# Performance work log

Measured on AMD Instinct MI355X. Metric: run time of the kernel, lower is better.

The kernel has to match this reference:

```python
import jax, jax.numpy as jnp
import numpy as np

H, KV, D = 12, 4, 128  # n_head, n_kv_head, head_dim
VE_GATE_CH = 12

def _rmsnorm(x):
    eps = jnp.finfo(x.dtype).eps  # matches torch F.rms_norm default eps
    return x * jax.lax.rsqrt(jnp.mean(x * x, axis=-1, keepdims=True) + eps)

def _rope(x, cos, sin):
    d = x.shape[-1] // 2
    x1, x2 = x[..., :d], x[..., d:]
    return jnp.concatenate([x1 * cos + x2 * sin, -x1 * sin + x2 * cos], axis=-1)

def setup_inputs() -> dict:
    key = jax.random.key(0)
    ks = jax.random.split(key, 9)
    B, T, C = 2, 2048, 1536
    x = jax.random.normal(ks[0], (B, T, C), jnp.float32)
    ve = jax.random.normal(ks[1], (B, T, KV * D), jnp.float32)
    ang = jax.random.uniform(ks[2], (1, T, 1, D // 2), jnp.float32) * (2.0 * np.pi)
    cos, sin = jnp.cos(ang), jnp.sin(ang)
    Wq = jax.random.normal(ks[3], (H * D, C), jnp.float32) * 0.02
    Wk = jax.random.normal(ks[4], (KV * D, C), jnp.float32) * 0.02
    Wv = jax.random.normal(ks[5], (KV * D, C), jnp.float32) * 0.02
    Wproj = jax.random.normal(ks[6], (C, C), jnp.float32) * 0.02
    Wg = jax.random.normal(ks[7], (KV, VE_GATE_CH), jnp.float32) * 0.02
    return dict(x=x, ve=ve, cos=cos, sin=sin, Wq=Wq, Wk=Wk, Wv=Wv, Wproj=Wproj, Wg=Wg, window=1024)

def reference(x, ve, cos, sin, Wq, Wk, Wv, Wproj, Wg, window):
    B, T, C = x.shape
    q = (x @ Wq.T).reshape(B, T, H, D)
    k = (x @ Wk.T).reshape(B, T, KV, D)
    v = (x @ Wv.T).reshape(B, T, KV, D)
    # value-embedding gate: 3*sigmoid(Linear(x[..., :12])) per kv head
    gate = 3.0 * jax.nn.sigmoid(x[..., :VE_GATE_CH] @ Wg.T)  # [B,T,KV]
    v = v + gate[..., None] * ve.reshape(B, T, KV, D)
    q = _rmsnorm(_rope(q, cos, sin)) * 1.2
    k = _rmsnorm(_rope(k, cos, sin)) * 1.2
    rep = H // KV  # GQA group size
    qh = q.transpose(0, 2, 1, 3).reshape(B, KV, rep, T, D)
    kh = k.transpose(0, 2, 1, 3)  # [B,KV,T,D]
    vh = v.transpose(0, 2, 1, 3)
    scores = jnp.einsum('bgrtd,bgsd->bgrts', qh, kh) / np.sqrt(D)
    row = jnp.arange(T)[:, None]
    col = jnp.arange(T)[None, :]
    if window < 0 or window >= T:
        mask = col <= row  # pure causal
    else:
        mask = (col <= row) & (row - col <= window)  # causal sliding window
    scores = jnp.where(mask, scores, -jnp.inf)
    att = jax.nn.softmax(scores, axis=-1)
    y = jnp.einsum('bgrts,bgsd->bgrtd', att, vh)
    y = y.reshape(B, H, T, D).transpose(0, 2, 1, 3).reshape(B, T, H * D)
    return y @ Wproj.T
```

## Files before the change

### kernel.cpp

```cpp
#include <hip/hip_runtime.h>
#include <hip/hip_bf16.h>
#include <math.h>

#define B_  2
#define T_  2048
#define C_  1536
#define H_  12
#define KV_ 4
#define D_  128
#define M_  (B_*T_)
#define REP_ (H_/KV_)
#define NQKV_ 2560

typedef __bf16 bf16x8 __attribute__((ext_vector_type(8)));
typedef float  f32x4  __attribute__((ext_vector_type(4)));
typedef unsigned u32x4 __attribute__((ext_vector_type(4)));

union BCast { u32x4 u; bf16x8 b; };

__device__ inline bf16x8 ldb8(const ushort* p) {
    BCast c; c.u = *reinterpret_cast<const u32x4*>(p); return c.b;
}

__device__ inline ushort f2bf(float f) {
    union { float f; unsigned u; } v; v.f = f;
    unsigned u = v.u;
    return (ushort)((u + 0x7FFF + ((u >> 16) & 1)) >> 16);
}

__device__ inline float bf2f(ushort u) {
    union { unsigned u; float f; } v; v.u = (unsigned)u << 16;
    return v.f;
}

__device__ inline void async_copy16(const ushort* g, ushort* l) {
    __builtin_amdgcn_global_load_lds(
        (const __attribute__((address_space(1))) unsigned*)g,
        (__attribute__((address_space(3))) unsigned*)l, 16, 0, 0);
}

__device__ __host__ inline int dperm(int d) {
    return (d < 32) ? d : (d < 64 ? d + 32 : (d < 96 ? d - 32 : d));
}

template<bool BF16OUT>
__global__ __launch_bounds__(256) void gemm_bf16_bt(const ushort* __restrict__ A,
                                                    const ushort* __restrict__ Bm,
                                                    void* __restrict__ Cp,
                                                    int M, int N, int K) {
    __shared__ ushort As[128 * 32];
    __shared__ ushort Bs[128 * 32];
    const int tid  = threadIdx.x;
    const int wave = tid >> 6, lane = tid & 63;
    const int m16 = lane & 15, quad = lane >> 4;
    const int bm = blockIdx.y * 128, bn = blockIdx.x * 128;
    const int wm = (wave >> 1) * 64, wn = (wave & 1) * 64;

    const int lrow = lane >> 2;
    const int lcol = (lane & 3) * 8;
    const ushort* Ag = A  + (size_t)(bm + wave * 16 + lrow) * K + lcol;
    const ushort* Bg = Bm + (size_t)(bn + wave * 16 + lrow) * K + lcol;
    ushort* AsW0 = As + wave * 512;
    ushort* AsW1 = As + 2048 + wave * 512;
    ushort* BsW0 = Bs + wave * 512;
    ushort* BsW1 = Bs + 2048 + wave * 512;
    const size_t rowskip = (size_t)64 * K;

    f32x4 acc[4][4];
    #pragma unroll
    for (int i = 0; i < 4; i++)
        #pragma unroll
        for (int j = 0; j < 4; j++) acc[i][j] = (f32x4){0.f, 0.f, 0.f, 0.f};

    for (int k0 = 0; k0 < K; k0 += 32) {
        async_copy16(Ag + k0,           AsW0);
        async_copy16(Ag + k0 + rowskip, AsW1);
        async_copy16(Bg + k0,           BsW0);
        async_copy16(Bg + k0 + rowskip, BsW1);
        __syncthreads();

        bf16x8 af[4], bfr[4];
        #pragma unroll
        for (int i = 0; i < 4; i++)
            af[i] = ldb8(As + (wm + i * 16 + m16) * 32 + quad * 8);
        #pragma unroll
        for (int j = 0; j < 4; j++)
            bfr[j] = ldb8(Bs + (wn + j * 16 + m16) * 32 + quad * 8);
        #pragma unroll
        for (int i = 0; i < 4; i++)
            #pragma unroll
            for (int j = 0; j < 4; j++)
                acc[i][j] = __builtin_amdgcn_mfma_f32_16x16x32_bf16(af[i], bfr[j], acc[i][j], 0, 0, 0);
        __syncthreads();
    }

    #pragma unroll
    for (int i = 0; i < 4; i++) {
        #pragma unroll
        for (int reg = 0; reg < 4; reg++) {
            const int row = bm + wm + i * 16 + quad * 4 + reg;
            if constexpr (BF16OUT) {
                ushort* C = (ushort*)Cp;
                #pragma unroll
                for (int j = 0; j < 4; j++)
                    C[(size_t)row * N + bn + wn + j * 16 + m16] = f2bf(acc[i][j][reg]);
            } else {
                float* C = (float*)Cp;
                #pragma unroll
                for (int j = 0; j < 4; j++)
                    C[(size_t)row * N + bn + wn + j * 16 + m16] = acc[i][j][reg];
            }
        }
    }
}

#define KQ_ 1536
__global__ __launch_bounds__(256) void gemm_qkv(const ushort* __restrict__ A,
                                                const ushort* __restrict__ Bm,
                                                ushort* __restrict__ Qp,
                                                ushort* __restrict__ Kp,
                                                ushort* __restrict__ vbuf,
                                                const float* __restrict__ cosb,
                                                const float* __restrict__ sinb) {
    __shared__ ushort As[128 * 32];
    __shared__ ushort Bs[128 * 32];
    const int tid  = threadIdx.x;
    const int wave = tid >> 6, lane = tid & 63;
    const int m16 = lane & 15, quad = lane >> 4;
    const int bm = blockIdx.y * 128, bn = blockIdx.x * 128;
    const int wm = (wave >> 1) * 64, wn = (wave & 1) * 64;

    const int lrow = lane >> 2;
    const int lcol = (lane & 3) * 8;
    const ushort* Ag = A  + (size_t)(bm + wave * 16 + lrow) * KQ_ + lcol;
    const ushort* Bg = Bm + (size_t)(bn + wave * 16 + lrow) * KQ_ + lcol;
    ushort* AsW0 = As + wave * 512;
    ushort* AsW1 = As + 2048 + wave * 512;
    ushort* BsW0 = Bs + wave * 512;
    ushort* BsW1 = Bs + 2048 + wave * 512;
    const size_t rowskip = (size_t)64 * KQ_;

    f32x4 acc[4][4];
    #pragma unroll
    for (int i = 0; i < 4; i++)
        #pragma unroll
        for (int j = 0; j < 4; j++) acc[i][j] = (f32x4){0.f, 0.f, 0.f, 0.f};

    for (int k0 = 0; k0 < KQ_; k0 += 32) {
        async_copy16(Ag + k0,           AsW0);
        async_copy16(Ag + k0 + rowskip, AsW1);
        async_copy16(Bg + k0,           BsW0);
        async_copy16(Bg + k0 + rowskip, BsW1);
        __syncthreads();

        bf16x8 af[4], bfr[4];
        #pragma unroll
        for (int i = 0; i < 4; i++)
            af[i] = ldb8(As + (wm + i * 16 + m16) * 32 + quad * 8);
        #pragma unroll
        for (int j = 0; j < 4; j++)
            bfr[j] = ldb8(Bs + (wn + j * 16 + m16) * 32 + quad * 8);
        #pragma unroll
        for (int i = 0; i < 4; i++)
            #pragma unroll
            for (int j = 0; j < 4; j++)
                acc[i][j] = __builtin_amdgcn_mfma_f32_16x16x32_bf16(af[i], bfr[j], acc[i][j], 0, 0, 0);
        __syncthreads();
    }

    if (bn < 2048) {
        float* ssqS = (float*)As;
        float ssq[4][4];
        #pragma unroll
        for (int i = 0; i < 4; i++) {
            #pragma unroll
            for (int reg = 0; reg < 4; reg++) {
                float v = acc[i][0][reg]*acc[i][0][reg] + acc[i][1][reg]*acc[i][1][reg]
                        + acc[i][2][reg]*acc[i][2][reg] + acc[i][3][reg]*acc[i][3][reg];
                v += __shfl_xor(v, 1); v += __shfl_xor(v, 2);
                v += __shfl_xor(v, 4); v += __shfl_xor(v, 8);
                ssq[i][reg] = v;
            }
        }
        if (m16 == 0) {
            #pragma unroll
            for (int i = 0; i < 4; i++)
                #pragma unroll
                for (int reg = 0; reg < 4; reg++)
                    ssqS[(wm + i*16 + quad*4 + reg) * 2 + (wave & 1)] = ssq[i][reg];
        }
        __syncthreads();

        const bool isq = (bn < 1536);
        const float osc = isq ? (1.2f * 1.2f * 0.08838834764831845f) : 1.0f;
        const int hh  = isq ? (bn >> 7) : ((bn - 1536) >> 7);
        const int nh  = isq ? H_ : KV_;
        ushort* outp  = isq ? Qp : Kp;

        float scl[4][4];
        #pragma unroll
        for (int i = 0; i < 4; i++) {
            #pragma unroll
            for (int reg = 0; reg < 4; reg++) {
                const int r = wm + i*16 + quad*4 + reg;
                const float tot = ssqS[r*2] + ssqS[r*2 + 1];
                scl[i][reg] = rsqrtf(tot * (1.0f/128.0f) + 1.1920928955078125e-07f) * osc;
            }
        }

        #pragma unroll
        for (int i = 0; i < 4; i++) {
            #pragma unroll
            for (int reg = 0; reg < 4; reg++) {
                const int row = bm + wm + i*16 + quad*4 + reg;
                const int b = row >> 11, t = row & (T_ - 1);
                ushort* orow = outp + ((size_t)(b * nh + hh) * T_ + t) * D_;
                const float sc = scl[i][reg];
                #pragma unroll
                for (int jp = 0; jp < 2; jp++) {
                    const int ipair = (wn ? 32 : 0) + jp*16 + m16;
                    const float c = cosb[t*64 + ipair], s = sinb[t*64 + ipair];
                    const float x1 = acc[i][jp][reg], x2 = acc[i][jp+2][reg];
                    orow[wn + jp*16 + m16]       = f2bf((x1*c + x2*s) * sc);
                    orow[wn + (jp+2)*16 + m16]   = f2bf((x2*c - x1*s) * sc);
                }
            }
        }
    } else {
        const int cb = bn - 2048 + wn;
        #pragma unroll
        for (int i = 0; i < 4; i++) {
            #pragma unroll
            for (int reg = 0; reg < 4; reg++) {
                const int row = bm + wm + i*16 + quad*4 + reg;
                ushort* vr = vbuf + (size_t)row * 512 + cb + m16;
                #pragma unroll
                for (int j = 0; j < 4; j++)
                    vr[j*16] = f2bf(acc[i][j][reg]);
            }
        }
    }
}

#define SEG0 1572864
#define SEG1 2162688
#define SEG2 2359296
#define SEG3 2555904
#define SEG4 3145728
#define ROW4 384
__global__ __launch_bounds__(256) void cast_all(const float* __restrict__ x,
                                                const float* __restrict__ Wq,
                                                const float* __restrict__ Wk,
                                                const float* __restrict__ Wv,
                                                const float* __restrict__ Wp,
                                                ushort* __restrict__ xb,
                                                ushort* __restrict__ Wqkvb,
                                                ushort* __restrict__ Wpb) {
    const int i = blockIdx.x * 256 + threadIdx.x;
    float4 v; size_t dst4; ushort* dstp;
    if (i < SEG0) {
        v = ((const float4*)x)[i]; dstp = xb; dst4 = i;
    } else if (i < SEG1) {
        const int j = i - SEG0;
        const int r = j / ROW4, c4 = j - r * ROW4;
        const int d = r & 127, hh = r >> 7;
        v = ((const float4*)Wq)[j]; dstp = Wqkvb;
        dst4 = (size_t)(hh * 128 + dperm(d)) * ROW4 + c4;
    } else if (i < SEG2) {
        const int j = i - SEG1;
        const int r = j / ROW4, c4 = j - r * ROW4;
        const int d = r & 127, g = r >> 7;
        v = ((const float4*)Wk)[j]; dstp = Wqkvb;
        dst4 = (size_t)(1536 + g * 128 + dperm(d)) * ROW4 + c4;
    } else if (i < SEG3) {
        const int j = i - SEG2;
        v = ((const float4*)Wv)[j]; dstp = Wqkvb;
        dst4 = (size_t)2048 * ROW4 + j;
    } else {
        const int j = i - SEG3;
        v = ((const float4*)Wp)[j]; dstp = Wpb; dst4 = j;
    }
    ((ushort4*)dstp)[dst4] = make_ushort4(f2bf(v.x), f2bf(v.y), f2bf(v.z), f2bf(v.w));
}

__global__ __launch_bounds__(256) void gate_vt(const ushort* __restrict__ vbuf,
                                               const float* __restrict__ x,
                                               const float* __restrict__ ve,
                                               const float* __restrict__ Wg,
                                               ushort* __restrict__ Vt) {
    const int t0 = blockIdx.x * 64, g = blockIdx.y, b = blockIdx.z;
    __shared__ float gateS[64];
    __shared__ ushort tile[128][66];
    const int tid = threadIdx.x;
    if (tid < 64) {
        const float* xr = x + (size_t)(b * T_ + t0 + tid) * C_;
        float acc = 0.f;
        #pragma unroll
        for (int c = 0; c < 12; c++) acc += xr[c] * Wg[g * 12 + c];
        gateS[tid] = 3.0f / (1.0f + __expf(-acc));
    }
    __syncthreads();
    #pragma unroll
    for (int i = 0; i < 32; i++) {
        int idx = i * 256 + tid;
        int r = idx >> 7;
        int d = idx & 127;
        size_t offv = (size_t)(b * T_ + t0 + r) * 512 + g * D_ + d;
        tile[d][r] = f2bf(bf2f(vbuf[offv]) + gateS[r] * ve[offv]);
    }
    __syncthreads();
    ushort* ob = Vt + ((size_t)(b * KV_ + g) * D_) * T_ + t0;
    #pragma unroll
    for (int i = 0; i < 32; i++) {
        int idx = i * 256 + tid;
        int d = idx >> 6;
        int c = idx & 63;
        ob[(size_t)d * T_ + c] = tile[d][c];
    }
}

__global__ __launch_bounds__(256, 3) void attn_mfma(const ushort* __restrict__ Qp,
                                                    const ushort* __restrict__ Kp,
                                                    const ushort* __restrict__ Vt,
                                                    ushort* __restrict__ Y,
                                                    const int* __restrict__ wptr) {
    const int t0 = blockIdx.x * 64;
    const int h  = blockIdx.y, b = blockIdx.z;
    const int g  = h / REP_;
    const int tid  = threadIdx.x;
    const int wave = tid >> 6, lane = tid & 63;
    const int m16 = lane & 15, quad = lane >> 4;

    __shared__ ushort Ks[4 * 32 * 32];
    __shared__ ushort Vs[128 * 32];
    __shared__ ushort Pl[4][16 * 40];

    const int w = *wptr;
    const bool windowed = (w >= 0 && w < T_);
    const unsigned wu = windowed ? (unsigned)w : 0x7FFFFFFFu;
    int s_lo = 0;
    if (windowed) { s_lo = t0 - w; if (s_lo < 0) s_lo = 0; }
    const int s_hi = t0 + 63;
    const int ss0 = s_lo & ~31;
    const int tw = t0 + wave * 16;

    const ushort* qrow = Qp + ((size_t)(b * H_ + h) * T_ + tw + m16) * D_ + quad * 8;
    bf16x8 qa[4];
    #pragma unroll
    for (int kc = 0; kc < 4; kc++) qa[kc] = ldb8(qrow + kc * 32);

    const ushort* kbase = Kp + (size_t)(b * KV_ + g) * T_ * D_;
    const ushort* vbase = Vt + (size_t)(b * KV_ + g) * D_ * T_;

    const int c0 = wave, c1 = wave + 4;
    const ushort* kg0 = kbase + (size_t)((c0 & 1) * 16 + (lane >> 2)) * D_ + (c0 >> 1) * 32 + (lane & 3) * 8;
    const ushort* kg1 = kbase + (size_t)((c1 & 1) * 16 + (lane >> 2)) * D_ + (c1 >> 1) * 32 + (lane & 3) * 8;
    ushort* kl0 = Ks + c0 * 512;
    ushort* kl1 = Ks + c1 * 512;
    const ushort* vg0 = vbase + (size_t)(c0 * 16 + (lane >> 2)) * T_ + (lane & 3) * 8;
    const ushort* vg1 = vbase + (size_t)(c1 * 16 + (lane >> 2)) * T_ + (lane & 3) * 8;
    ushort* vl0 = Vs + c0 * 512;
    ushort* vl1 = Vs + c1 * 512;

    f32x4 o[8];
    #pragma unroll
    for (int dt = 0; dt < 8; dt++) o[dt] = (f32x4){0.f, 0.f, 0.f, 0.f};
    f32x4 lacc = (f32x4){0.f, 0.f, 0.f, 0.f};
    BCast onesc; onesc.u = (u32x4){0x3F803F80u, 0x3F803F80u, 0x3F803F80u, 0x3F803F80u};
    const bf16x8 ones = onesc.b;
    ushort* pw = &Pl[wave][0];

    for (int ss = ss0; ss <= s_hi; ss += 32) {
        const size_t koff = (size_t)ss * D_;
        async_copy16(kg0 + koff, kl0);
        async_copy16(kg1 + koff, kl1);
        async_copy16(vg0 + ss,   vl0);
        async_copy16(vg1 + ss,   vl1);
        __syncthreads();

        f32x4 s0 = (f32x4){0.f,0.f,0.f,0.f};
        f32x4 s1 = (f32x4){0.f,0.f,0.f,0.f};
        #pragma unroll
        for (int kc = 0; kc < 4; kc++) {
            bf16x8 kf0 = ldb8(Ks + kc * 1024 + m16 * 32 + quad * 8);
            bf16x8 kf1 = ldb8(Ks + kc * 1024 + (16 + m16) * 32 + quad * 8);
            s0 = __builtin_amdgcn_mfma_f32_16x16x32_bf16(qa[kc], kf0, s0, 0, 0, 0);
            s1 = __builtin_amdgcn_mfma_f32_16x16x32_bf16(qa[kc], kf1, s1, 0, 0, 0);
        }

        const int sA = ss + m16, sB = ss + 16 + m16;
        #pragma unroll
        for (int reg = 0; reg < 4; reg++) {
            const int t = tw + quad * 4 + reg;
            const float pa = ((unsigned)(t - sA) <= wu) ? __expf(s0[reg]) : 0.f;
            const float pb = ((unsigned)(t - sB) <= wu) ? __expf(s1[reg]) : 0.f;
            pw[(quad * 4 + reg) * 40 + m16]      = f2bf(pa);
            pw[(quad * 4 + reg) * 40 + 16 + m16] = f2bf(pb);
        }

        __builtin_amdgcn_s_waitcnt(0xc07f);
        bf16x8 pfrag = ldb8(pw + m16 * 40 + quad * 8);

        #pragma unroll
        for (int dt = 0; dt < 8; dt++) {
            bf16x8 vf = ldb8(Vs + (dt * 16 + m16) * 32 + quad * 8);
            o[dt] = __builtin_amdgcn_mfma_f32_16x16x32_bf16(pfrag, vf, o[dt], 0, 0, 0);
        }
        lacc = __builtin_amdgcn_mfma_f32_16x16x32_bf16(pfrag, ones, lacc, 0, 0, 0);
        __syncthreads();
    }

    float inv[4];
    #pragma unroll
    for (int reg = 0; reg < 4; reg++) inv[reg] = 1.0f / lacc[reg];
    ushort* yb = Y + ((size_t)(b * T_ + tw + quad * 4) * H_ + h) * D_ + m16;
    #pragma unroll
    for (int reg = 0; reg < 4; reg++)
        #pragma unroll
        for (int dt = 0; dt < 8; dt++)
            yb[(size_t)reg * H_ * D_ + dt * 16] = f2bf(o[dt][reg] * inv[reg]);
}

extern "C" void kernel_launch(void* const* d_in, const int* in_sizes, int n_in,
                              void* d_out, int out_size, void* d_ws, size_t ws_size,
                              hipStream_t stream) {
    const float* x     = (const float*)d_in[0];
    const float* ve    = (const float*)d_in[1];
    const float* cosb  = (const float*)d_in[2];
    const float* sinb  = (const float*)d_in[3];
    const float* Wq    = (const float*)d_in[4];
    const float* Wk    = (const float*)d_in[5];
    const float* Wv    = (const float*)d_in[6];
    const float* Wproj = (const float*)d_in[7];
    const float* Wg    = (const float*)d_in[8];
    const int*   wptr  = (const int*)d_in[9];
    float* out = (float*)d_out;

    ushort* xb    = (ushort*)d_ws;
    ushort* vbuf  = xb    + (size_t)M_ * C_;
    ushort* Qp    = vbuf  + (size_t)M_ * 512;
    ushort* Kp    = Qp    + (size_t)M_ * C_;
    ushort* Vt    = Kp    + (size_t)M_ * 512;
    ushort* yb16  = Vt    + (size_t)M_ * 512;
    ushort* Wqkvb = yb16  + (size_t)M_ * C_;
    ushort* Wpb   = Wqkvb + (size_t)NQKV_ * C_;

    cast_all<<<SEG4 / 256, 256, 0, stream>>>(x, Wq, Wk, Wv, Wproj, xb, Wqkvb, Wpb);

    gemm_qkv<<<dim3(NQKV_ / 128, M_ / 128), 256, 0, stream>>>(xb, Wqkvb, Qp, Kp, vbuf,
                                                              cosb, sinb);

    gate_vt<<<dim3(T_ / 64, KV_, B_), 256, 0, stream>>>(vbuf, x, ve, Wg, Vt);

    attn_mfma<<<dim3(T_ / 64, H_, B_), 256, 0, stream>>>(Qp, Kp, Vt, yb16, wptr);

    gemm_bf16_bt<false><<<dim3(C_ / 128, M_ / 128), 256, 0, stream>>>(yb16, Wpb, out, M_, C_, C_);
}
```

Measured before the change: 277.5 us.

## Move RoPE/RMSNorm out of QKV GEMM epilogue and double attention query tile

The QKV GEMM now writes raw bf16 Q and K without the row-norm reduction, barrier and RoPE in its epilogue. A new small kernel applies RoPE and RMSNorm to K in place. The attention kernel applies them to Q while loading it. Each attention wave now handles 32 query rows instead of 16, so every K/V tile staged in LDS is reused across twice the rows, with half the blocks. The costs are an extra launch plus a read-modify-write pass over K, Q normalization done on bf16-rounded values, and higher register pressure (launch bounds lowered from 3 to 2 blocks per SM).

Result: slower. 291.8 us (+5.1%).

```diff
diff --git a/kernel.cpp b/kernel.cpp
--- a/kernel.cpp
+++ b/kernel.cpp
@@ -16,7 +16,7 @@
 typedef float  f32x4  __attribute__((ext_vector_type(4)));
 typedef unsigned u32x4 __attribute__((ext_vector_type(4)));
 
-union BCast { u32x4 u; bf16x8 b; };
+union BCast { u32x4 u; bf16x8 b; ushort s[8]; };
 
 __device__ inline bf16x8 ldb8(const ushort* p) {
     BCast c; c.u = *reinterpret_cast<const u32x4*>(p); return c.b;
@@ -119,9 +119,7 @@
                                                 const ushort* __restrict__ Bm,
                                                 ushort* __restrict__ Qp,
                                                 ushort* __restrict__ Kp,
-                                                ushort* __restrict__ vbuf,
-                                                const float* __restrict__ cosb,
-                                                const float* __restrict__ sinb) {
+                                                ushort* __restrict__ vbuf) {
     __shared__ ushort As[128 * 32];
     __shared__ ushort Bs[128 * 32];
     const int tid  = threadIdx.x;
@@ -169,61 +167,20 @@
     }
 
     if (bn < 2048) {
-        float* ssqS = (float*)As;
-        float ssq[4][4];
+        const bool isq = (bn < 1536);
+        const int hh = isq ? (bn >> 7) : ((bn - 1536) >> 7);
+        const int nh = isq ? H_ : KV_;
+        ushort* outp = isq ? Qp : Kp;
         #pragma unroll
         for (int i = 0; i < 4; i++) {
             #pragma unroll
             for (int reg = 0; reg < 4; reg++) {
-                float v = acc[i][0][reg]*acc[i][0][reg] + acc[i][1][reg]*acc[i][1][reg]
-                        + acc[i][2][reg]*acc[i][2][reg] + acc[i][3][reg]*acc[i][3][reg];
-                v += __shfl_xor(v, 1); v += __shfl_xor(v, 2);
-                v += __shfl_xor(v, 4); v += __shfl_xor(v, 8);
-                ssq[i][reg] = v;
-            }
-        }
-        if (m16 == 0) {
-            #pragma unroll
-            for (int i = 0; i < 4; i++)
+                const int row = bm + wm + i * 16 + quad * 4 + reg;
+                const int b = row >> 11, t = row & (T_ - 1);
+                ushort* orow = outp + ((size_t)(b * nh + hh) * T_ + t) * D_ + wn + m16;
                 #pragma unroll
-                for (int reg = 0; reg < 4; reg++)
-                    ssqS[(wm + i*16 + quad*4 + reg) * 2 + (wave & 1)] = ssq[i][reg];
-        }
-        __syncthreads();
-
-        const bool isq = (bn < 1536);
-        const float osc = isq ? (1.2f * 1.2f * 0.08838834764831845f) : 1.0f;
-        const int hh  = isq ? (bn >> 7) : ((bn - 1536) >> 7);
-        const int nh  = isq ? H_ : KV_;
-        ushort* outp  = isq ? Qp : Kp;
-
-        float scl[4][4];
-        #pragma unroll
-        for (int i = 0; i < 4; i++) {
-            #pragma unroll
-            for (int reg = 0; reg < 4; reg++) {
-                const int r = wm + i*16 + quad*4 + reg;
-                const float tot = ssqS[r*2] + ssqS[r*2 + 1];
-                scl[i][reg] = rsqrtf(tot * (1.0f/128.0f) + 1.1920928955078125e-07f) * osc;
-            }
-        }
-
-        #pragma unroll
-        for (int i = 0; i < 4; i++) {
-            #pragma unroll
-            for (int reg = 0; reg < 4; reg++) {
-                const int row = bm + wm + i*16 + quad*4 + reg;
-                const int b = row >> 11, t = row & (T_ - 1);
-                ushort* orow = outp + ((size_t)(b * nh + hh) * T_ + t) * D_;
-                const float sc = scl[i][reg];
-                #pragma unroll
-                for (int jp = 0; jp < 2; jp++) {
-                    const int ipair = (wn ? 32 : 0) + jp*16 + m16;
-                    const float c = cosb[t*64 + ipair], s = sinb[t*64 + ipair];
-                    const float x1 = acc[i][jp][reg], x2 = acc[i][jp+2][reg];
-                    orow[wn + jp*16 + m16]       = f2bf((x1*c + x2*s) * sc);
-                    orow[wn + (jp+2)*16 + m16]   = f2bf((x2*c - x1*s) * sc);
-                }
+                for (int j = 0; j < 4; j++)
+                    orow[j * 16] = f2bf(acc[i][j][reg]);
             }
         }
     } else {
@@ -232,11 +189,11 @@
         for (int i = 0; i < 4; i++) {
             #pragma unroll
             for (int reg = 0; reg < 4; reg++) {
-                const int row = bm + wm + i*16 + quad*4 + reg;
+                const int row = bm + wm + i * 16 + quad * 4 + reg;
                 ushort* vr = vbuf + (size_t)row * 512 + cb + m16;
                 #pragma unroll
                 for (int j = 0; j < 4; j++)
-                    vr[j*16] = f2bf(acc[i][j][reg]);
+                    vr[j * 16] = f2bf(acc[i][j][reg]);
             }
         }
     }
@@ -283,6 +240,24 @@
     ((ushort4*)dstp)[dst4] = make_ushort4(f2bf(v.x), f2bf(v.y), f2bf(v.z), f2bf(v.w));
 }
 
+__global__ __launch_bounds__(256) void rope_rms_k(ushort* __restrict__ Kp,
+                                                  const float* __restrict__ cosb,
+                                                  const float* __restrict__ sinb) {
+    const int row = blockIdx.x * 4 + (threadIdx.x >> 6);
+    const int t = row & (T_ - 1);
+    ushort* p = Kp + (size_t)row * D_;
+    const int L = threadIdx.x & 63;
+    const int pp = (L < 32) ? L : L + 32;
+    const float c = cosb[t * 64 + L], s = sinb[t * 64 + L];
+    const float x1 = bf2f(p[pp]), x2 = bf2f(p[pp + 32]);
+    float ssq = x1 * x1 + x2 * x2;
+    #pragma unroll
+    for (int off = 32; off > 0; off >>= 1) ssq += __shfl_xor(ssq, off);
+    const float scale = rsqrtf(ssq * (1.0f / 128.0f) + 1.1920928955078125e-07f);
+    p[pp]      = f2bf((x1 * c + x2 * s) * scale);
+    p[pp + 32] = f2bf((x2 * c - x1 * s) * scale);
+}
+
 __global__ __launch_bounds__(256) void gate_vt(const ushort* __restrict__ vbuf,
                                                const float* __restrict__ x,
                                                const float* __restrict__ ve,
@@ -319,12 +294,14 @@
     }
 }
 
-__global__ __launch_bounds__(256, 3) void attn_mfma(const ushort* __restrict__ Qp,
+__global__ __launch_bounds__(256, 2) void attn_mfma(const ushort* __restrict__ Qp,
                                                     const ushort* __restrict__ Kp,
                                                     const ushort* __restrict__ Vt,
                                                     ushort* __restrict__ Y,
-                                                    const int* __restrict__ wptr) {
-    const int t0 = blockIdx.x * 64;
+                                                    const int* __restrict__ wptr,
+                                                    const float* __restrict__ cosb,
+                                                    const float* __restrict__ sinb) {
+    const int t0 = blockIdx.x * 128;
     const int h  = blockIdx.y, b = blockIdx.z;
     const int g  = h / REP_;
     const int tid  = threadIdx.x;
@@ -333,21 +310,51 @@
 
     __shared__ ushort Ks[4 * 32 * 32];
     __shared__ ushort Vs[128 * 32];
-    __shared__ ushort Pl[4][16 * 40];
+    __shared__ ushort Pl[4][32 * 40];
 
     const int w = *wptr;
     const bool windowed = (w >= 0 && w < T_);
     const unsigned wu = windowed ? (unsigned)w : 0x7FFFFFFFu;
     int s_lo = 0;
     if (windowed) { s_lo = t0 - w; if (s_lo < 0) s_lo = 0; }
-    const int s_hi = t0 + 63;
+    const int s_hi = t0 + 127;
     const int ss0 = s_lo & ~31;
-    const int tw = t0 + wave * 16;
-
-    const ushort* qrow = Qp + ((size_t)(b * H_ + h) * T_ + tw + m16) * D_ + quad * 8;
-    bf16x8 qa[4];
-    #pragma unroll
-    for (int kc = 0; kc < 4; kc++) qa[kc] = ldb8(qrow + kc * 32);
+    const int tw = t0 + wave * 32;
+
+    bf16x8 qa[2][4];
+    #pragma unroll
+    for (int mt = 0; mt < 2; mt++) {
+        const int t = tw + mt * 16 + m16;
+        const ushort* qrow = Qp + ((size_t)(b * H_ + h) * T_ + t) * D_ + quad * 8;
+        float qf[4][8];
+        float ssq = 0.f;
+        #pragma unroll
+        for (int kc = 0; kc < 4; kc++) {
+            BCast c; c.u = *reinterpret_cast<const u32x4*>(qrow + kc * 32);
+            #pragma unroll
+            for (int j = 0; j < 8; j++) {
+                const float f = bf2f(c.s[j]);
+                qf[kc][j] = f; ssq += f * f;
+            }
+        }
+        ssq += __shfl_xor(ssq, 16);
+        ssq += __shfl_xor(ssq, 32);
+        const float scale = rsqrtf(ssq * (1.0f / 128.0f) + 1.1920928955078125e-07f)
+                          * (1.2f * 1.2f * 0.08838834764831845f);
+        const float* cb = cosb + t * 64 + quad * 8;
+        const float* sb = sinb + t * 64 + quad * 8;
+        BCast o0, o1, o2, o3;
+        #pragma unroll
+        for (int j = 0; j < 8; j++) {
+            const float c0 = cb[j],      s0 = sb[j];
+            const float c1 = cb[32 + j], s1 = sb[32 + j];
+            o0.s[j] = f2bf((qf[0][j] * c0 + qf[1][j] * s0) * scale);
+            o1.s[j] = f2bf((qf[1][j] * c0 - qf[0][j] * s0) * scale);
+            o2.s[j] = f2bf((qf[2][j] * c1 + qf[3][j] * s1) * scale);
+            o3.s[j] = f2bf((qf[3][j] * c1 - qf[2][j] * s1) * scale);
+        }
+        qa[mt][0] = o0.b; qa[mt][1] = o1.b; qa[mt][2] = o2.b; qa[mt][3] = o3.b;
+    }
 
     const ushort* kbase = Kp + (size_t)(b * KV_ + g) * T_ * D_;
     const ushort* vbase = Vt + (size_t)(b * KV_ + g) * D_ * T_;
@@ -362,10 +369,14 @@
     ushort* vl0 = Vs + c0 * 512;
     ushort* vl1 = Vs + c1 * 512;
 
-    f32x4 o[8];
-    #pragma unroll
-    for (int dt = 0; dt < 8; dt++) o[dt] = (f32x4){0.f, 0.f, 0.f, 0.f};
-    f32x4 lacc = (f32x4){0.f, 0.f, 0.f, 0.f};
+    f32x4 o[2][8];
+    f32x4 lacc[2];
+    #pragma unroll
+    for (int mt = 0; mt < 2; mt++) {
+        lacc[mt] = (f32x4){0.f, 0.f, 0.f, 0.f};
+        #pragma unroll
+        for (int dt = 0; dt < 8; dt++) o[mt][dt] = (f32x4){0.f, 0.f, 0.f, 0.f};
+    }
     BCast onesc; onesc.u = (u32x4){0x3F803F80u, 0x3F803F80u, 0x3F803F80u, 0x3F803F80u};
     const bf16x8 ones = onesc.b;
     ushort* pw = &Pl[wave][0];
@@ -378,47 +389,62 @@
         async_copy16(vg1 + ss,   vl1);
         __syncthreads();
 
-        f32x4 s0 = (f32x4){0.f,0.f,0.f,0.f};
-        f32x4 s1 = (f32x4){0.f,0.f,0.f,0.f};
+        f32x4 sc[2][2];
+        #pragma unroll
+        for (int mt = 0; mt < 2; mt++)
+            #pragma unroll
+            for (int hf = 0; hf < 2; hf++) sc[mt][hf] = (f32x4){0.f,0.f,0.f,0.f};
         #pragma unroll
         for (int kc = 0; kc < 4; kc++) {
             bf16x8 kf0 = ldb8(Ks + kc * 1024 + m16 * 32 + quad * 8);
             bf16x8 kf1 = ldb8(Ks + kc * 1024 + (16 + m16) * 32 + quad * 8);
-            s0 = __builtin_amdgcn_mfma_f32_16x16x32_bf16(qa[kc], kf0, s0, 0, 0, 0);
-            s1 = __builtin_amdgcn_mfma_f32_16x16x32_bf16(qa[kc], kf1, s1, 0, 0, 0);
-        }
-
-        const int sA = ss + m16, sB = ss + 16 + m16;
-        #pragma unroll
-        for (int reg = 0; reg < 4; reg++) {
-            const int t = tw + quad * 4 + reg;
-            const float pa = ((unsigned)(t - sA) <= wu) ? __expf(s0[reg]) : 0.f;
-            const float pb = ((unsigned)(t - sB) <= wu) ? __expf(s1[reg]) : 0.f;
-            pw[(quad * 4 + reg) * 40 + m16]      = f2bf(pa);
-            pw[(quad * 4 + reg) * 40 + 16 + m16] = f2bf(pb);
+            sc[0][0] = __builtin_amdgcn_mfma_f32_16x16x32_bf16(qa[0][kc], kf0, sc[0][0], 0, 0, 0);
+            sc[0][1] = __builtin_amdgcn_mfma_f32_16x16x32_bf16(qa[0][kc], kf1, sc[0][1], 0, 0, 0);
+            sc[1][0] = __builtin_amdgcn_mfma_f32_16x16x32_bf16(qa[1][kc], kf0, sc[1][0], 0, 0, 0);
+            sc[1][1] = __builtin_amdgcn_mfma_f32_16x16x32_bf16(qa[1][kc], kf1, sc[1][1], 0, 0, 0);
+        }
+
+        #pragma unroll
+        for (int mt = 0; mt < 2; mt++) {
+            #pragma unroll
+            for (int hf = 0; hf < 2; hf++) {
+                const int sA = ss + hf * 16 + m16;
+                #pragma unroll
+                for (int reg = 0; reg < 4; reg++) {
+                    const int t = tw + mt * 16 + quad * 4 + reg;
+                    const float p = ((unsigned)(t - sA) <= wu) ? __expf(sc[mt][hf][reg]) : 0.f;
+                    pw[(mt * 16 + quad * 4 + reg) * 40 + hf * 16 + m16] = f2bf(p);
+                }
+            }
         }
 
         __builtin_amdgcn_s_waitcnt(0xc07f);
-        bf16x8 pfrag = ldb8(pw + m16 * 40 + quad * 8);
+        bf16x8 pf0 = ldb8(pw + m16 * 40 + quad * 8);
+        bf16x8 pf1 = ldb8(pw + (16 + m16) * 40 + quad * 8);
 
         #pragma unroll
         for (int dt = 0; dt < 8; dt++) {
             bf16x8 vf = ldb8(Vs + (dt * 16 + m16) * 32 + quad * 8);
-            o[dt] = __builtin_amdgcn_mfma_f32_16x16x32_bf16(pfrag, vf, o[dt], 0, 0, 0);
-        }
-        lacc = __builtin_amdgcn_mfma_f32_16x16x32_bf16(pfrag, ones, lacc, 0, 0, 0);
-        __syncthreads();
-    }
-
-    float inv[4];
-    #pragma unroll
-    for (int reg = 0; reg < 4; reg++) inv[reg] = 1.0f / lacc[reg];
-    ushort* yb = Y + ((size_t)(b * T_ + tw + quad * 4) * H_ + h) * D_ + m16;
-    #pragma unroll
-    for (int reg = 0; reg < 4; reg++)
-        #pragma unroll
-        for (int dt = 0; dt < 8; dt++)
-            yb[(size_t)reg * H_ * D_ + dt * 16] = f2bf(o[dt][reg] * inv[reg]);
+            o[0][dt] = __builtin_amdgcn_mfma_f32_16x16x32_bf16(pf0, vf, o[0][dt], 0, 0, 0);
+            o[1][dt] = __builtin_amdgcn_mfma_f32_16x16x32_bf16(pf1, vf, o[1][dt], 0, 0, 0);
+        }
+        lacc[0] = __builtin_amdgcn_mfma_f32_16x16x32_bf16(pf0, ones, lacc[0], 0, 0, 0);
+        lacc[1] = __builtin_amdgcn_mfma_f32_16x16x32_bf16(pf1, ones, lacc[1], 0, 0, 0);
+        __syncthreads();
+    }
+
+    #pragma unroll
+    for (int mt = 0; mt < 2; mt++) {
+        float inv[4];
+        #pragma unroll
+        for (int reg = 0; reg < 4; reg++) inv[reg] = 1.0f / lacc[mt][reg];
+        ushort* yb = Y + ((size_t)(b * T_ + tw + mt * 16 + quad * 4) * H_ + h) * D_ + m16;
+        #pragma unroll
+        for (int reg = 0; reg < 4; reg++)
+            #pragma unroll
+            for (int dt = 0; dt < 8; dt++)
+                yb[(size_t)reg * H_ * D_ + dt * 16] = f2bf(o[mt][dt][reg] * inv[reg]);
+    }
 }
 
 extern "C" void kernel_launch(void* const* d_in, const int* in_sizes, int n_in,
@@ -447,12 +473,13 @@
 
     cast_all<<<SEG4 / 256, 256, 0, stream>>>(x, Wq, Wk, Wv, Wproj, xb, Wqkvb, Wpb);
 
-    gemm_qkv<<<dim3(NQKV_ / 128, M_ / 128), 256, 0, stream>>>(xb, Wqkvb, Qp, Kp, vbuf,
-                                                              cosb, sinb);
+    gemm_qkv<<<dim3(NQKV_ / 128, M_ / 128), 256, 0, stream>>>(xb, Wqkvb, Qp, Kp, vbuf);
+
+    rope_rms_k<<<M_ * KV_ / 4, 256, 0, stream>>>(Kp, cosb, sinb);
 
     gate_vt<<<dim3(T_ / 64, KV_, B_), 256, 0, stream>>>(vbuf, x, ve, Wg, Vt);
 
-    attn_mfma<<<dim3(T_ / 64, H_, B_), 256, 0, stream>>>(Qp, Kp, Vt, yb16, wptr);
+    attn_mfma<<<dim3(T_ / 128, H_, B_), 256, 0, stream>>>(Qp, Kp, Vt, yb16, wptr, cosb, sinb);
 
     gemm_bf16_bt<false><<<dim3(C_ / 128, M_ / 128), 256, 0, stream>>>(yb16, Wpb, out, M_, C_, C_);
 }
```
